# Kernel tuning notes

Measured on AMD Instinct MI355X. Metric: run time of the kernel, lower is better.

Reference implementation:

```python
import jax, jax.numpy as jnp
import numpy as np

N, E = 100000, 1600000
IN_C, OUT_C, H, EDGE_DIM = 128, 64, 2, 4
NEG_SLOPE = 0.2
LN_EPS = 1e-5


def setup_inputs() -> dict:
    key = jax.random.key(0)
    ks = jax.random.split(key, 12)
    s = 1.0 / np.sqrt(IN_C)
    inp = {
        "x": jax.random.normal(ks[0], (N, IN_C), jnp.float32),
        "edge_index": jax.random.randint(ks[1], (2, E), 0, N, jnp.int64),
        "edge_attr": jax.random.normal(ks[2], (E, EDGE_DIM), jnp.float32),
        "W": jax.random.normal(ks[3], (IN_C, H * OUT_C), jnp.float32) * s,
        "att_src": jax.random.normal(ks[4], (H, OUT_C), jnp.float32) * s,
        "att_dst": jax.random.normal(ks[5], (H, OUT_C), jnp.float32) * s,
        "W_edge": jax.random.normal(ks[6], (EDGE_DIM, H * OUT_C), jnp.float32) * 0.5,
        "att_edge": jax.random.normal(ks[7], (H, OUT_C), jnp.float32) * s,
        "bias": jnp.zeros((OUT_C,), jnp.float32),
        "gamma": jnp.ones((OUT_C,), jnp.float32),
        "beta": jnp.zeros((OUT_C,), jnp.float32),
    }
    return inp


def reference(x, edge_index, edge_attr, W, att_src, att_dst, W_edge, att_edge, bias, gamma, beta):
    n = x.shape[0]
    src, dst = edge_index[0], edge_index[1]
    # shared src/dst linear (PyG GATConv with single input tensor)
    h = (x @ W).reshape(n, H, OUT_C)                       # [N,H,C]
    a_src = jnp.einsum("nhc,hc->nh", h, att_src)          # [N,H]
    a_dst = jnp.einsum("nhc,hc->nh", h, att_dst)          # [N,H]
    e = (edge_attr @ W_edge).reshape(-1, H, OUT_C)         # [E,H,C]
    a_edge = jnp.einsum("ehc,hc->eh", e, att_edge)        # [E,H]
    alpha = jax.nn.leaky_relu(a_src[src] + a_dst[dst] + a_edge, NEG_SLOPE)  # [E,H]
    # segment softmax over edges grouped by destination node
    amax = jax.ops.segment_max(alpha, dst, num_segments=n)
    ex = jnp.exp(alpha - amax[dst])
    denom = jax.ops.segment_sum(ex, dst, num_segments=n)
    w = ex / (denom[dst] + 1e-16)                          # [E,H]
    msg = h[src] * w[:, :, None]                           # [E,H,C]
    out = jax.ops.segment_sum(msg, dst, num_segments=n)    # [N,H,C]
    out = out.mean(axis=1) + bias                          # concat=False -> head mean
    # LayerNorm + ReLU
    mu = out.mean(-1, keepdims=True)
    var = ((out - mu) ** 2).mean(-1, keepdims=True)
    out = (out - mu) * jax.lax.rsqrt(var + LN_EPS) * gamma + beta
    return jax.nn.relu(out)
```

## Files before the change

kernel.cpp:

```cpp
#include <hip/hip_runtime.h>
#include <hip/hip_fp16.h>
#include <math.h>

#define IN_C 128
#define HC   128
#define OUT_C 64
#define NEG_SLOPE 0.2f
#define LN_EPS 1e-5f
#define CHUNK 4096
#define BSH   8
#define BMSK  255
#define NBMAX 512
#define NB2MAX 1024

typedef __attribute__((ext_vector_type(8))) _Float16 f16x8;
typedef __attribute__((ext_vector_type(4))) float f32x4;

__device__ inline unsigned h2pack(float a, float b) {
    __half2 h = __floats2half2_rn(a, b);
    return *reinterpret_cast<unsigned*>(&h);
}

__global__ __launch_bounds__(256) void k_pre(const float* __restrict__ W,
                                             const float* __restrict__ W_edge,
                                             const float* __restrict__ att_edge,
                                             const int* __restrict__ ei_dst,
                                             unsigned short* __restrict__ WhT,
                                             float* __restrict__ V,
                                             int* __restrict__ off,
                                             int E, int NB, int PB) {
    __shared__ int hist[NBMAX];
    int b = blockIdx.x, t = threadIdx.x;
    if (b < 8) {
        #pragma unroll
        for (int i = 0; i < 8; ++i) {
            int idx = b * 2048 + i * 256 + t;
            int k = idx >> 7, col = idx & 127;
            __half hh = __float2half_rn(W[idx]);
            WhT[col * 128 + k] = *reinterpret_cast<unsigned short*>(&hh);
        }
        return;
    }
    if (b == 8) {
        if (t < 8) {
            int d = t >> 1, h = t & 1;
            float s = 0.f;
            for (int c = 0; c < 64; ++c)
                s += W_edge[d * HC + h * 64 + c] * att_edge[h * 64 + c];
            V[d * 2 + h] = s;
        }
        return;
    }
    int pb = b - 9;
    for (int i = t; i < NB; i += 256) hist[i] = 0;
    __syncthreads();
    int base = pb * CHUNK;
    int lim = E - base; if (lim > CHUNK) lim = CHUNK;
    if (lim == CHUNK) {
        #pragma unroll
        for (int u = 0; u < 4; ++u) {
            int4 v = *(const int4*)&ei_dst[base + u * 1024 + t * 4];
            atomicAdd(&hist[v.x >> BSH], 1);
            atomicAdd(&hist[v.y >> BSH], 1);
            atomicAdd(&hist[v.z >> BSH], 1);
            atomicAdd(&hist[v.w >> BSH], 1);
        }
    } else {
        for (int i = t; i < lim; i += 256)
            atomicAdd(&hist[ei_dst[base + i] >> BSH], 1);
    }
    __syncthreads();
    for (int i = t; i < NB; i += 256)
        off[(size_t)i * PB + pb] = hist[i];
}

__global__ __launch_bounds__(256) void k_scan(int* __restrict__ off,
                                              int* __restrict__ bsum, int nS) {
    __shared__ int sm[256];
    int t = threadIdx.x;
    int base = blockIdx.x * 1024 + t * 4;
    int v0 = 0, v1 = 0, v2 = 0, v3 = 0;
    if (base + 0 < nS) v0 = off[base + 0];
    if (base + 1 < nS) v1 = off[base + 1];
    if (base + 2 < nS) v2 = off[base + 2];
    if (base + 3 < nS) v3 = off[base + 3];
    int s = v0 + v1 + v2 + v3;
    sm[t] = s;
    __syncthreads();
    for (int o = 1; o < 256; o <<= 1) {
        int u = (t >= o) ? sm[t - o] : 0;
        __syncthreads();
        sm[t] += u;
        __syncthreads();
    }
    int excl = sm[t] - s;
    if (base + 0 < nS) off[base + 0] = excl;
    if (base + 1 < nS) off[base + 1] = excl + v0;
    if (base + 2 < nS) off[base + 2] = excl + v0 + v1;
    if (base + 3 < nS) off[base + 3] = excl + v0 + v1 + v2;
    if (t == 255) bsum[blockIdx.x] = sm[255];
}

__device__ inline void scan_bsum(const int* __restrict__ bsum, int nb2,
                                 int* bs, int* sm, int t) {
    int v0 = (4 * t + 0 < nb2) ? bsum[4 * t + 0] : 0;
    int v1 = (4 * t + 1 < nb2) ? bsum[4 * t + 1] : 0;
    int v2 = (4 * t + 2 < nb2) ? bsum[4 * t + 2] : 0;
    int v3 = (4 * t + 3 < nb2) ? bsum[4 * t + 3] : 0;
    int s = v0 + v1 + v2 + v3;
    sm[t] = s;
    __syncthreads();
    for (int o = 1; o < 256; o <<= 1) {
        int u = (t >= o) ? sm[t - o] : 0;
        __syncthreads();
        sm[t] += u;
        __syncthreads();
    }
    int excl = sm[t] - s;
    bs[4 * t + 0] = excl;
    bs[4 * t + 1] = excl + v0;
    bs[4 * t + 2] = excl + v0 + v1;
    bs[4 * t + 3] = excl + v0 + v1 + v2;
    __syncthreads();
}

__global__ __launch_bounds__(256) void k_fused(
        const float* __restrict__ x,
        const unsigned short* __restrict__ WhT,
        const float* __restrict__ attS, const float* __restrict__ attD,
        unsigned* __restrict__ hb,
        float* __restrict__ a_src, float* __restrict__ a_dst, int M,
        const int* __restrict__ ei, const float* __restrict__ ea,
        const float* __restrict__ V,
        const int* __restrict__ off, const int* __restrict__ bsum,
        int* __restrict__ bsum2, uint2* __restrict__ pA,
        int E, int NB, int PB, int nb2, int GB) {
    __shared__ unsigned xb[64 * 64];
    const int t = threadIdx.x;
    const int bid = blockIdx.x;
    const int r5 = bid % 5, g5 = bid / 5;

    if (r5 == 4) {
        int* cur = (int*)xb;
        int* bs  = (int*)xb + NBMAX;
        int* sm  = (int*)xb + NBMAX + NB2MAX;
        int pb = g5;
        scan_bsum(bsum, nb2, bs, sm, t);
        if (pb == 0)
            for (int i = t; i < nb2; i += 256) bsum2[i] = bs[i];
        for (int i = t; i < NB; i += 256) {
            size_t oi = (size_t)i * PB + pb;
            cur[i] = off[oi] + bs[(int)(oi >> 10)];
        }
        __syncthreads();
        float v0 = V[0], v1 = V[1], v2 = V[2], v3 = V[3];
        float v4 = V[4], v5 = V[5], v6 = V[6], v7 = V[7];
        int base = pb * CHUNK;
        int lim = E - base; if (lim > CHUNK) lim = CHUNK;
        if (lim == CHUNK) {
            #pragma unroll
            for (int h = 0; h < 2; ++h) {
                int e0 = base + h * 2048 + t;
                int sA[8], dA[8];
                #pragma unroll
                for (int k = 0; k < 8; ++k) {
                    sA[k] = ei[e0 + k * 256];
                    dA[k] = ei[E + e0 + k * 256];
                }
                float4 aA[8];
                #pragma unroll
                for (int k = 0; k < 8; ++k)
                    aA[k] = ((const float4*)ea)[e0 + k * 256];
                #pragma unroll
                for (int k = 0; k < 8; ++k) {
                    float ae0 = aA[k].x * v0 + aA[k].y * v2 + aA[k].z * v4 + aA[k].w * v6;
                    float ae1 = aA[k].x * v1 + aA[k].y * v3 + aA[k].z * v5 + aA[k].w * v7;
                    int slot = atomicAdd(&cur[dA[k] >> BSH], 1);
                    pA[slot] = make_uint2(
                        (unsigned)sA[k] | ((unsigned)(dA[k] & BMSK) << 17),
                        h2pack(ae0, ae1));
                }
            }
        } else {
            for (int i = t; i < lim; i += 256) {
                int e = base + i;
                int s = ei[e], d = ei[E + e];
                float4 a = ((const float4*)ea)[e];
                float ae0 = a.x * v0 + a.y * v2 + a.z * v4 + a.w * v6;
                float ae1 = a.x * v1 + a.y * v3 + a.z * v5 + a.w * v7;
                int slot = atomicAdd(&cur[d >> BSH], 1);
                pA[slot] = make_uint2((unsigned)s | ((unsigned)(d & BMSK) << 17),
                                      h2pack(ae0, ae1));
            }
        }
        return;
    }

    const int gid = g5 * 4 + r5;
    if (gid >= GB) return;
    const int brow = gid * 64;
    const float4* x4 = (const float4*)x;
    #pragma unroll
    for (int i = 0; i < 8; ++i) {
        int idx = i * 256 + t;
        int row = idx >> 5, c4 = idx & 31;
        float4 v = make_float4(0.f, 0.f, 0.f, 0.f);
        if (brow + row < M) v = x4[(size_t)(brow + row) * 32 + c4];
        unsigned lo = h2pack(v.x, v.y), hi = h2pack(v.z, v.w);
        int byte = row * 256 + ((c4 * 8) ^ ((row & 7) << 4));
        *(uint2*)((char*)xb + byte) = make_uint2(lo, hi);
    }
    __syncthreads();

    const int w = t >> 6, lane = t & 63;
    const int col = lane & 15, qr = lane >> 4;
    f32x4 acc[8];
    #pragma unroll
    for (int ct = 0; ct < 8; ++ct) acc[ct] = (f32x4){0.f, 0.f, 0.f, 0.f};

    const int arow = w * 16 + col;
    #pragma unroll
    for (int ks = 0; ks < 4; ++ks) {
        int abyte = arow * 256 + ((ks * 64 + qr * 16) ^ ((arow & 7) << 4));
        f16x8 af = *(const f16x8*)((const char*)xb + abyte);
        #pragma unroll
        for (int ct = 0; ct < 8; ++ct) {
            f16x8 bfr = *(const f16x8*)&WhT[(size_t)(ct * 16 + col) * 128 + ks * 32 + qr * 8];
            acc[ct] = __builtin_amdgcn_mfma_f32_16x16x32_f16(af, bfr, acc[ct], 0, 0, 0);
        }
    }

    float pS0[4], pS1[4], pD0[4], pD1[4];
    #pragma unroll
    for (int r = 0; r < 4; ++r) { pS0[r] = pS1[r] = pD0[r] = pD1[r] = 0.f; }
    #pragma unroll
    for (int ct = 0; ct < 8; ++ct) {
        float s = attS[ct * 16 + col], d = attD[ct * 16 + col];
        #pragma unroll
        for (int r = 0; r < 4; ++r) {
            float a = acc[ct][r];
            if (ct < 4) { pS0[r] += a * s; pD0[r] += a * d; }
            else        { pS1[r] += a * s; pD1[r] += a * d; }
        }
    }
    #pragma unroll
    for (int m = 1; m < 16; m <<= 1) {
        #pragma unroll
        for (int r = 0; r < 4; ++r) {
            pS0[r] += __shfl_xor(pS0[r], m);
            pS1[r] += __shfl_xor(pS1[r], m);
            pD0[r] += __shfl_xor(pD0[r], m);
            pD1[r] += __shfl_xor(pD1[r], m);
        }
    }
    #pragma unroll
    for (int r = 0; r < 4; ++r) {
        int grow = brow + w * 16 + qr * 4 + r;
        if (grow < M) {
            if (col == 0) {
                a_src[2 * grow + 0] = pS0[r];
                a_src[2 * grow + 1] = pS1[r];
                a_dst[2 * grow + 0] = pD0[r];
                a_dst[2 * grow + 1] = pD1[r];
            }
            #pragma unroll
            for (int ct = 0; ct < 4; ++ct)
                hb[(size_t)grow * 64 + ct * 16 + col] =
                    h2pack(acc[ct][r], acc[ct + 4][r]);
        }
    }
}

__global__ __launch_bounds__(256) void k_csr(const uint2* __restrict__ pA,
                                             const int* __restrict__ off,
                                             const int* __restrict__ bsum2,
                                             const float* __restrict__ a_src,
                                             const float* __restrict__ a_dst,
                                             int* __restrict__ rowptr,
                                             uint2* __restrict__ payload,
                                             int M, int E, int NB, int PB) {
    __shared__ int cnt[256];
    __shared__ int sc[256];
    __shared__ int cur[256];
    __shared__ float2 adl[256];
    int b = blockIdx.x, t = threadIdx.x;
    int n0 = b << BSH;
    int nloc = M - n0; if (nloc > 256) nloc = 256;

    size_t o0 = (size_t)b * PB;
    int s0 = off[o0] + bsum2[(int)(o0 >> 10)];
    int s1 = E;
    if (b + 1 < NB) {
        size_t o1 = (size_t)(b + 1) * PB;
        s1 = off[o1] + bsum2[(int)(o1 >> 10)];
    }
    cnt[t] = 0;
    if (t < nloc) adl[t] = ((const float2*)a_dst)[n0 + t];
    __syncthreads();

    for (int i = s0 + t; i < s1; i += 256)
        atomicAdd(&cnt[(pA[i].x >> 17) & BMSK], 1);
    __syncthreads();
    int c = cnt[t];
    sc[t] = c;
    __syncthreads();
    for (int o = 1; o < 256; o <<= 1) {
        int u = (t >= o) ? sc[t - o] : 0;
        __syncthreads();
        sc[t] += u;
        __syncthreads();
    }
    {
        int base = s0 + sc[t] - c;
        cur[t] = base;
        if (t < nloc) rowptr[n0 + t] = base;
    }
    if (b == NB - 1 && t == 0) rowptr[M] = E;
    __syncthreads();
    for (int i = s0 + t; i < s1; i += 256) {
        uint2 p = pA[i];
        int src = p.x & 0x1FFFF;
        int dl = (p.x >> 17) & BMSK;
        __half2 aeh = *reinterpret_cast<__half2*>(&p.y);
        float2 as = ((const float2*)a_src)[src];
        float2 ad = adl[dl];
        float al0 = as.x + ad.x + __low2float(aeh);
        al0 = al0 > 0.f ? al0 : NEG_SLOPE * al0;
        float al1 = as.y + ad.y + __high2float(aeh);
        al1 = al1 > 0.f ? al1 : NEG_SLOPE * al1;
        int pos = atomicAdd(&cur[dl], 1);
        payload[pos] = make_uint2((unsigned)src,
                                  h2pack(__expf(al0), __expf(al1)));
    }
}

__global__ __launch_bounds__(256) void k_gather(const uint2* __restrict__ payload,
                                                const int* __restrict__ rowptr,
                                                const unsigned* __restrict__ hb,
                                                const float* __restrict__ bias,
                                                const float* __restrict__ gamma,
                                                const float* __restrict__ beta,
                                                float* __restrict__ out, int M) {
    __shared__ uint2 stg[4][64];
    int w = threadIdx.x >> 6, lane = threadIdx.x & 63;
    int n = blockIdx.x * 4 + w;
    if (n >= M) return;
    int beg = rowptr[n], end = rowptr[n + 1];
    float acc0 = 0.f, acc1 = 0.f, pe0 = 0.f, pe1 = 0.f;

    for (int base = beg; base < end; base += 64) {
        int cnt = end - base; if (cnt > 64) cnt = 64;
        uint2 p = make_uint2(0u, 0u);
        if (lane < cnt) p = payload[base + lane];
        stg[w][lane] = p;
        {
            __half2 he = *reinterpret_cast<__half2*>(&p.y);
            pe0 += __low2float(he);
            pe1 += __high2float(he);
        }
        int j = 0;
        for (; j + 8 <= cnt; j += 8) {
            uint2 q0 = stg[w][j + 0], q1 = stg[w][j + 1];
            uint2 q2 = stg[w][j + 2], q3 = stg[w][j + 3];
            uint2 q4 = stg[w][j + 4], q5 = stg[w][j + 5];
            uint2 q6 = stg[w][j + 6], q7 = stg[w][j + 7];
            int s0 = __builtin_amdgcn_readfirstlane((int)q0.x);
            int s1 = __builtin_amdgcn_readfirstlane((int)q1.x);
            int s2 = __builtin_amdgcn_readfirstlane((int)q2.x);
            int s3 = __builtin_amdgcn_readfirstlane((int)q3.x);
            int s4 = __builtin_amdgcn_readfirstlane((int)q4.x);
            int s5 = __builtin_amdgcn_readfirstlane((int)q5.x);
            int s6 = __builtin_amdgcn_readfirstlane((int)q6.x);
            int s7 = __builtin_amdgcn_readfirstlane((int)q7.x);
            unsigned h0 = (hb + (size_t)s0 * 64)[lane];
            unsigned h1 = (hb + (size_t)s1 * 64)[lane];
            unsigned h2 = (hb + (size_t)s2 * 64)[lane];
            unsigned h3 = (hb + (size_t)s3 * 64)[lane];
            unsigned h4 = (hb + (size_t)s4 * 64)[lane];
            unsigned h5 = (hb + (size_t)s5 * 64)[lane];
            unsigned h6 = (hb + (size_t)s6 * 64)[lane];
            unsigned h7 = (hb + (size_t)s7 * 64)[lane];
            __half2 e0 = *reinterpret_cast<__half2*>(&q0.y);
            __half2 e1 = *reinterpret_cast<__half2*>(&q1.y);
            __half2 e2 = *reinterpret_cast<__half2*>(&q2.y);
            __half2 e3 = *reinterpret_cast<__half2*>(&q3.y);
            __half2 e4 = *reinterpret_cast<__half2*>(&q4.y);
            __half2 e5 = *reinterpret_cast<__half2*>(&q5.y);
            __half2 e6 = *reinterpret_cast<__half2*>(&q6.y);
            __half2 e7 = *reinterpret_cast<__half2*>(&q7.y);
            __half2 g0 = *reinterpret_cast<__half2*>(&h0);
            __half2 g1 = *reinterpret_cast<__half2*>(&h1);
            __half2 g2 = *reinterpret_cast<__half2*>(&h2);
            __half2 g3 = *reinterpret_cast<__half2*>(&h3);
            __half2 g4 = *reinterpret_cast<__half2*>(&h4);
            __half2 g5 = *reinterpret_cast<__half2*>(&h5);
            __half2 g6 = *reinterpret_cast<__half2*>(&h6);
            __half2 g7 = *reinterpret_cast<__half2*>(&h7);
            acc0 += __low2float(e0)  * __low2float(g0);
            acc1 += __high2float(e0) * __high2float(g0);
            acc0 += __low2float(e1)  * __low2float(g1);
            acc1 += __high2float(e1) * __high2float(g1);
            acc0 += __low2float(e2)  * __low2float(g2);
            acc1 += __high2float(e2) * __high2float(g2);
            acc0 += __low2float(e3)  * __low2float(g3);
            acc1 += __high2float(e3) * __high2float(g3);
            acc0 += __low2float(e4)  * __low2float(g4);
            acc1 += __high2float(e4) * __high2float(g4);
            acc0 += __low2float(e5)  * __low2float(g5);
            acc1 += __high2float(e5) * __high2float(g5);
            acc0 += __low2float(e6)  * __low2float(g6);
            acc1 += __high2float(e6) * __high2float(g6);
            acc0 += __low2float(e7)  * __low2float(g7);
            acc1 += __high2float(e7) * __high2float(g7);
        }
        for (; j + 4 <= cnt; j += 4) {
            uint2 q0 = stg[w][j + 0], q1 = stg[w][j + 1];
            uint2 q2 = stg[w][j + 2], q3 = stg[w][j + 3];
            int s0 = __builtin_amdgcn_readfirstlane((int)q0.x);
            int s1 = __builtin_amdgcn_readfirstlane((int)q1.x);
            int s2 = __builtin_amdgcn_readfirstlane((int)q2.x);
            int s3 = __builtin_amdgcn_readfirstlane((int)q3.x);
            unsigned h0 = (hb + (size_t)s0 * 64)[lane];
            unsigned h1 = (hb + (size_t)s1 * 64)[lane];
            unsigned h2 = (hb + (size_t)s2 * 64)[lane];
            unsigned h3 = (hb + (size_t)s3 * 64)[lane];
            __half2 e0 = *reinterpret_cast<__half2*>(&q0.y);
            __half2 e1 = *reinterpret_cast<__half2*>(&q1.y);
            __half2 e2 = *reinterpret_cast<__half2*>(&q2.y);
            __half2 e3 = *reinterpret_cast<__half2*>(&q3.y);
            __half2 g0 = *reinterpret_cast<__half2*>(&h0);
            __half2 g1 = *reinterpret_cast<__half2*>(&h1);
            __half2 g2 = *reinterpret_cast<__half2*>(&h2);
            __half2 g3 = *reinterpret_cast<__half2*>(&h3);
            acc0 += __low2float(e0)  * __low2float(g0);
            acc1 += __high2float(e0) * __high2float(g0);
            acc0 += __low2float(e1)  * __low2float(g1);
            acc1 += __high2float(e1) * __high2float(g1);
            acc0 += __low2float(e2)  * __low2float(g2);
            acc1 += __high2float(e2) * __high2float(g2);
            acc0 += __low2float(e3)  * __low2float(g3);
            acc1 += __high2float(e3) * __high2float(g3);
        }
        for (; j < cnt; ++j) {
            uint2 q0 = stg[w][j];
            int s0 = __builtin_amdgcn_readfirstlane((int)q0.x);
            unsigned h0 = (hb + (size_t)s0 * 64)[lane];
            __half2 e0 = *reinterpret_cast<__half2*>(&q0.y);
            __half2 g0 = *reinterpret_cast<__half2*>(&h0);
            acc0 += __low2float(e0)  * __low2float(g0);
            acc1 += __high2float(e0) * __high2float(g0);
        }
    }

    float d0 = pe0, d1 = pe1;
    #pragma unroll
    for (int m = 32; m; m >>= 1) {
        d0 += __shfl_xor(d0, m);
        d1 += __shfl_xor(d1, m);
    }

    float o = 0.5f * (acc0 / (d0 + 1e-16f) + acc1 / (d1 + 1e-16f)) + bias[lane];
    float mu = o;
    #pragma unroll
    for (int m = 32; m; m >>= 1) mu += __shfl_xor(mu, m);
    mu *= (1.f / 64.f);
    float c = o - mu;
    float v = c * c;
    #pragma unroll
    for (int m = 32; m; m >>= 1) v += __shfl_xor(v, m);
    v *= (1.f / 64.f);
    float y = c * rsqrtf(v + LN_EPS) * gamma[lane] + beta[lane];
    out[(size_t)n * OUT_C + lane] = fmaxf(y, 0.f);
}

extern "C" void kernel_launch(void* const* d_in, const int* in_sizes, int n_in,
                              void* d_out, int out_size, void* d_ws, size_t ws_size,
                              hipStream_t stream) {
    const float* x     = (const float*)d_in[0];
    const int*   ei    = (const int*)d_in[1];
    const float* ea    = (const float*)d_in[2];
    const float* W     = (const float*)d_in[3];
    const float* attS  = (const float*)d_in[4];
    const float* attD  = (const float*)d_in[5];
    const float* We    = (const float*)d_in[6];
    const float* attE  = (const float*)d_in[7];
    const float* bias  = (const float*)d_in[8];
    const float* gamma = (const float*)d_in[9];
    const float* beta  = (const float*)d_in[10];

    const int M  = in_sizes[0] / IN_C;
    const int E  = in_sizes[1] / 2;
    const int NB = (M + BMSK) >> BSH;
    const int PB = (E + CHUNK - 1) / CHUNK;
    const int nS = NB * PB;
    const int nb2 = (nS + 1023) / 1024;
    const int GB = (M + 63) / 64;

    char* ws = (char*)d_ws;
    size_t woff = 0;
    auto alloc = [&](size_t bytes) -> void* {
        void* p = ws + woff;
        woff += (bytes + 255) & ~(size_t)255;
        return p;
    };
    unsigned*       hb     = (unsigned*)      alloc((size_t)M * 64 * 4);
    float*          a_src  = (float*)         alloc((size_t)M * 2 * 4);
    float*          a_dst  = (float*)         alloc((size_t)M * 2 * 4);
    int*            off    = (int*)           alloc((size_t)nS * 4);
    int*            bsum   = (int*)           alloc((size_t)nb2 * 4);
    int*            bsum2  = (int*)           alloc((size_t)nb2 * 4);
    int*            rowptr = (int*)           alloc((size_t)(M + 1) * 4);
    uint2*          pA     = (uint2*)         alloc((size_t)E * 8);
    uint2*          payload= (uint2*)         alloc((size_t)E * 8);
    unsigned short* WhT    = (unsigned short*)alloc(128 * 128 * 2);
    float*          V      = (float*)         alloc(32);

    k_pre<<<9 + PB, 256, 0, stream>>>(W, We, attE, ei + E, WhT, V, off, E, NB, PB);
    k_scan<<<nb2, 256, 0, stream>>>(off, bsum, nS);
    k_fused<<<5 * PB, 256, 0, stream>>>(x, WhT, attS, attD, hb, a_src, a_dst, M,
                                        ei, ea, V, off, bsum, bsum2, pA,
                                        E, NB, PB, nb2, GB);
    k_csr<<<NB, 256, 0, stream>>>(pA, off, bsum2, a_src, a_dst, rowptr, payload,
                                  M, E, NB, PB);
    k_gather<<<(M + 3) / 4, 256, 0, stream>>>(payload, rowptr, hb, bias, gamma, beta,
                                              (float*)d_out, M);
}
```

Measured before the change: 143.8 us.

## Precompute attention logits via folded W·att vectors in k_pre; move exp to scatter

Folds att_src/att_dst into W to get four 128-length vectors, and computes a_src/a_dst per node directly from fp32 x inside the histogram kernel. The partition stage of k_fused then gathers a_src/a_dst and stores exp(leaky_relu(logit)) in the payload. k_csr becomes a plain permute without random a_src reads. This moves the random gather earlier and cuts the reduction epilogue from the MFMA path, at the cost of an extra full read of x in k_pre and random a_src/a_dst gathers in the scatter pass.

```diff
diff --git a/kernel.cpp b/kernel.cpp
--- a/kernel.cpp
+++ b/kernel.cpp
@@ -24,12 +24,18 @@
 __global__ __launch_bounds__(256) void k_pre(const float* __restrict__ W,
                                              const float* __restrict__ W_edge,
                                              const float* __restrict__ att_edge,
+                                             const float* __restrict__ attS,
+                                             const float* __restrict__ attD,
+                                             const float* __restrict__ x,
                                              const int* __restrict__ ei_dst,
                                              unsigned short* __restrict__ WhT,
                                              float* __restrict__ V,
                                              int* __restrict__ off,
-                                             int E, int NB, int PB) {
+                                             float* __restrict__ a_src,
+                                             float* __restrict__ a_dst,
+                                             int E, int M, int NB, int PB) {
     __shared__ int hist[NBMAX];
+    __shared__ float wsv0[128], wsv1[128], wdv0[128], wdv1[128];
     int b = blockIdx.x, t = threadIdx.x;
     if (b < 8) {
         #pragma unroll
@@ -52,26 +58,63 @@
         return;
     }
     int pb = b - 9;
+
     for (int i = t; i < NB; i += 256) hist[i] = 0;
-    __syncthreads();
-    int base = pb * CHUNK;
-    int lim = E - base; if (lim > CHUNK) lim = CHUNK;
-    if (lim == CHUNK) {
-        #pragma unroll
-        for (int u = 0; u < 4; ++u) {
-            int4 v = *(const int4*)&ei_dst[base + u * 1024 + t * 4];
-            atomicAdd(&hist[v.x >> BSH], 1);
-            atomicAdd(&hist[v.y >> BSH], 1);
-            atomicAdd(&hist[v.z >> BSH], 1);
-            atomicAdd(&hist[v.w >> BSH], 1);
-        }
-    } else {
-        for (int i = t; i < lim; i += 256)
-            atomicAdd(&hist[ei_dst[base + i] >> BSH], 1);
-    }
-    __syncthreads();
-    for (int i = t; i < NB; i += 256)
-        off[(size_t)i * PB + pb] = hist[i];
+    if (t < 128) {
+        const float* wr = W + t * 128;
+        float s0 = 0.f, s1 = 0.f, d0 = 0.f, d1 = 0.f;
+        for (int c = 0; c < 64; ++c) {
+            float w0 = wr[c], w1 = wr[64 + c];
+            s0 += w0 * attS[c];      s1 += w1 * attS[64 + c];
+            d0 += w0 * attD[c];      d1 += w1 * attD[64 + c];
+        }
+        wsv0[t] = s0; wsv1[t] = s1; wdv0[t] = d0; wdv1[t] = d1;
+    }
+    __syncthreads();
+
+    if (pb < PB) {
+        int base = pb * CHUNK;
+        int lim = E - base; if (lim > CHUNK) lim = CHUNK;
+        if (lim == CHUNK) {
+            #pragma unroll
+            for (int u = 0; u < 4; ++u) {
+                int4 v = *(const int4*)&ei_dst[base + u * 1024 + t * 4];
+                atomicAdd(&hist[v.x >> BSH], 1);
+                atomicAdd(&hist[v.y >> BSH], 1);
+                atomicAdd(&hist[v.z >> BSH], 1);
+                atomicAdd(&hist[v.w >> BSH], 1);
+            }
+        } else {
+            for (int i = t; i < lim; i += 256)
+                atomicAdd(&hist[ei_dst[base + i] >> BSH], 1);
+        }
+    }
+    {
+        int n = pb * 256 + t;
+        if (pb < NB && n < M) {
+            const float4* xr4 = (const float4*)(x + (size_t)n * 128);
+            float s0 = 0.f, s1 = 0.f, d0 = 0.f, d1 = 0.f;
+            #pragma unroll 8
+            for (int q = 0; q < 32; ++q) {
+                float4 xv = xr4[q];
+                int k = q * 4;
+                s0 += xv.x * wsv0[k]     + xv.y * wsv0[k + 1]
+                    + xv.z * wsv0[k + 2] + xv.w * wsv0[k + 3];
+                s1 += xv.x * wsv1[k]     + xv.y * wsv1[k + 1]
+                    + xv.z * wsv1[k + 2] + xv.w * wsv1[k + 3];
+                d0 += xv.x * wdv0[k]     + xv.y * wdv0[k + 1]
+                    + xv.z * wdv0[k + 2] + xv.w * wdv0[k + 3];
+                d1 += xv.x * wdv1[k]     + xv.y * wdv1[k + 1]
+                    + xv.z * wdv1[k + 2] + xv.w * wdv1[k + 3];
+            }
+            ((float2*)a_src)[n] = make_float2(s0, s1);
+            ((float2*)a_dst)[n] = make_float2(d0, d1);
+        }
+    }
+    __syncthreads();
+    if (pb < PB)
+        for (int i = t; i < NB; i += 256)
+            off[(size_t)i * PB + pb] = hist[i];
 }
 
 __global__ __launch_bounds__(256) void k_scan(int* __restrict__ off,
@@ -127,11 +170,10 @@
 __global__ __launch_bounds__(256) void k_fused(
         const float* __restrict__ x,
         const unsigned short* __restrict__ WhT,
-        const float* __restrict__ attS, const float* __restrict__ attD,
-        unsigned* __restrict__ hb,
-        float* __restrict__ a_src, float* __restrict__ a_dst, int M,
+        unsigned* __restrict__ hb, int M,
         const int* __restrict__ ei, const float* __restrict__ ea,
         const float* __restrict__ V,
+        const float* __restrict__ a_src, const float* __restrict__ a_dst,
         const int* __restrict__ off, const int* __restrict__ bsum,
         int* __restrict__ bsum2, uint2* __restrict__ pA,
         int E, int NB, int PB, int nb2, int GB) {
@@ -171,14 +213,24 @@
                 #pragma unroll
                 for (int k = 0; k < 8; ++k)
                     aA[k] = ((const float4*)ea)[e0 + k * 256];
+                float2 asA[8], adA[8];
+                #pragma unroll
+                for (int k = 0; k < 8; ++k) {
+                    asA[k] = ((const float2*)a_src)[sA[k]];
+                    adA[k] = ((const float2*)a_dst)[dA[k]];
+                }
                 #pragma unroll
                 for (int k = 0; k < 8; ++k) {
                     float ae0 = aA[k].x * v0 + aA[k].y * v2 + aA[k].z * v4 + aA[k].w * v6;
                     float ae1 = aA[k].x * v1 + aA[k].y * v3 + aA[k].z * v5 + aA[k].w * v7;
+                    float al0 = asA[k].x + adA[k].x + ae0;
+                    al0 = al0 > 0.f ? al0 : NEG_SLOPE * al0;
+                    float al1 = asA[k].y + adA[k].y + ae1;
+                    al1 = al1 > 0.f ? al1 : NEG_SLOPE * al1;
                     int slot = atomicAdd(&cur[dA[k] >> BSH], 1);
                     pA[slot] = make_uint2(
                         (unsigned)sA[k] | ((unsigned)(dA[k] & BMSK) << 17),
-                        h2pack(ae0, ae1));
+                        h2pack(__expf(al0), __expf(al1)));
                 }
             }
         } else {
@@ -188,9 +240,13 @@
                 float4 a = ((const float4*)ea)[e];
                 float ae0 = a.x * v0 + a.y * v2 + a.z * v4 + a.w * v6;
                 float ae1 = a.x * v1 + a.y * v3 + a.z * v5 + a.w * v7;
+                float2 as = ((const float2*)a_src)[s];
+                float2 ad = ((const float2*)a_dst)[d];
+                float al0 = as.x + ad.x + ae0; al0 = al0 > 0.f ? al0 : NEG_SLOPE * al0;
+                float al1 = as.y + ad.y + ae1; al1 = al1 > 0.f ? al1 : NEG_SLOPE * al1;
                 int slot = atomicAdd(&cur[d >> BSH], 1);
                 pA[slot] = make_uint2((unsigned)s | ((unsigned)(d & BMSK) << 17),
-                                      h2pack(ae0, ae1));
+                                      h2pack(__expf(al0), __expf(al1)));
             }
         }
         return;
@@ -230,39 +286,10 @@
         }
     }
 
-    float pS0[4], pS1[4], pD0[4], pD1[4];
-    #pragma unroll
-    for (int r = 0; r < 4; ++r) { pS0[r] = pS1[r] = pD0[r] = pD1[r] = 0.f; }
-    #pragma unroll
-    for (int ct = 0; ct < 8; ++ct) {
-        float s = attS[ct * 16 + col], d = attD[ct * 16 + col];
-        #pragma unroll
-        for (int r = 0; r < 4; ++r) {
-            float a = acc[ct][r];
-            if (ct < 4) { pS0[r] += a * s; pD0[r] += a * d; }
-            else        { pS1[r] += a * s; pD1[r] += a * d; }
-        }
-    }
-    #pragma unroll
-    for (int m = 1; m < 16; m <<= 1) {
-        #pragma unroll
-        for (int r = 0; r < 4; ++r) {
-            pS0[r] += __shfl_xor(pS0[r], m);
-            pS1[r] += __shfl_xor(pS1[r], m);
-            pD0[r] += __shfl_xor(pD0[r], m);
-            pD1[r] += __shfl_xor(pD1[r], m);
-        }
-    }
     #pragma unroll
     for (int r = 0; r < 4; ++r) {
         int grow = brow + w * 16 + qr * 4 + r;
         if (grow < M) {
-            if (col == 0) {
-                a_src[2 * grow + 0] = pS0[r];
-                a_src[2 * grow + 1] = pS1[r];
-                a_dst[2 * grow + 0] = pD0[r];
-                a_dst[2 * grow + 1] = pD1[r];
-            }
             #pragma unroll
             for (int ct = 0; ct < 4; ++ct)
                 hb[(size_t)grow * 64 + ct * 16 + col] =
@@ -274,15 +301,12 @@
 __global__ __launch_bounds__(256) void k_csr(const uint2* __restrict__ pA,
                                              const int* __restrict__ off,
                                              const int* __restrict__ bsum2,
-                                             const float* __restrict__ a_src,
-                                             const float* __restrict__ a_dst,
                                              int* __restrict__ rowptr,
                                              uint2* __restrict__ payload,
                                              int M, int E, int NB, int PB) {
     __shared__ int cnt[256];
     __shared__ int sc[256];
     __shared__ int cur[256];
-    __shared__ float2 adl[256];
     int b = blockIdx.x, t = threadIdx.x;
     int n0 = b << BSH;
     int nloc = M - n0; if (nloc > 256) nloc = 256;
@@ -295,7 +319,6 @@
         s1 = off[o1] + bsum2[(int)(o1 >> 10)];
     }
     cnt[t] = 0;
-    if (t < nloc) adl[t] = ((const float2*)a_dst)[n0 + t];
     __syncthreads();
 
     for (int i = s0 + t; i < s1; i += 256)
@@ -319,18 +342,9 @@
     __syncthreads();
     for (int i = s0 + t; i < s1; i += 256) {
         uint2 p = pA[i];
-        int src = p.x & 0x1FFFF;
         int dl = (p.x >> 17) & BMSK;
-        __half2 aeh = *reinterpret_cast<__half2*>(&p.y);
-        float2 as = ((const float2*)a_src)[src];
-        float2 ad = adl[dl];
-        float al0 = as.x + ad.x + __low2float(aeh);
-        al0 = al0 > 0.f ? al0 : NEG_SLOPE * al0;
-        float al1 = as.y + ad.y + __high2float(aeh);
-        al1 = al1 > 0.f ? al1 : NEG_SLOPE * al1;
         int pos = atomicAdd(&cur[dl], 1);
-        payload[pos] = make_uint2((unsigned)src,
-                                  h2pack(__expf(al0), __expf(al1)));
+        payload[pos] = make_uint2(p.x & 0x1FFFF, p.y);
     }
 }
 
@@ -495,6 +509,7 @@
     const int nS = NB * PB;
     const int nb2 = (nS + 1023) / 1024;
     const int GB = (M + 63) / 64;
+    const int PREB = (PB > NB ? PB : NB);
 
     char* ws = (char*)d_ws;
     size_t woff = 0;
@@ -515,13 +530,12 @@
     unsigned short* WhT    = (unsigned short*)alloc(128 * 128 * 2);
     float*          V      = (float*)         alloc(32);
 
-    k_pre<<<9 + PB, 256, 0, stream>>>(W, We, attE, ei + E, WhT, V, off, E, NB, PB);
+    k_pre<<<9 + PREB, 256, 0, stream>>>(W, We, attE, attS, attD, x, ei + E,
+                                        WhT, V, off, a_src, a_dst, E, M, NB, PB);
     k_scan<<<nb2, 256, 0, stream>>>(off, bsum, nS);
-    k_fused<<<5 * PB, 256, 0, stream>>>(x, WhT, attS, attD, hb, a_src, a_dst, M,
-                                        ei, ea, V, off, bsum, bsum2, pA,
-                                        E, NB, PB, nb2, GB);
-    k_csr<<<NB, 256, 0, stream>>>(pA, off, bsum2, a_src, a_dst, rowptr, payload,
-                                  M, E, NB, PB);
+    k_fused<<<5 * PB, 256, 0, stream>>>(x, WhT, hb, M, ei, ea, V, a_src, a_dst,
+                                        off, bsum, bsum2, pA, E, NB, PB, nb2, GB);
+    k_csr<<<NB, 256, 0, stream>>>(pA, off, bsum2, rowptr, payload, M, E, NB, PB);
     k_gather<<<(M + 3) / 4, 256, 0, stream>>>(payload, rowptr, hb, bias, gamma, beta,
                                               (float*)d_out, M);
 }
```

Measured after the change: 173.9 us. +20.9%, slower.

## Fuse offset scan with GEMM kernel and compute attention exp during partition

Applied to the files above, without the earlier changes.

The chunk-offset scan now runs as extra blocks inside the node GEMM kernel, and the edge partition becomes its own kernel launched after it. Because a_src and a_dst are then ready, the partition computes the leaky-relu and exp of the attention logit and stores it in the payload. The CSR kernel only copies the payload instead of gathering a_src per edge. This removes one launch and moves the random a_src gather to a phase with better memory-level parallelism, but it loses the overlap of partitioning with the GEMM and adds random a_dst reads.

```diff
diff --git a/kernel.cpp b/kernel.cpp
--- a/kernel.cpp
+++ b/kernel.cpp
@@ -74,131 +74,48 @@
         off[(size_t)i * PB + pb] = hist[i];
 }
 
-__global__ __launch_bounds__(256) void k_scan(int* __restrict__ off,
-                                              int* __restrict__ bsum, int nS) {
-    __shared__ int sm[256];
-    int t = threadIdx.x;
-    int base = blockIdx.x * 1024 + t * 4;
-    int v0 = 0, v1 = 0, v2 = 0, v3 = 0;
-    if (base + 0 < nS) v0 = off[base + 0];
-    if (base + 1 < nS) v1 = off[base + 1];
-    if (base + 2 < nS) v2 = off[base + 2];
-    if (base + 3 < nS) v3 = off[base + 3];
-    int s = v0 + v1 + v2 + v3;
-    sm[t] = s;
-    __syncthreads();
-    for (int o = 1; o < 256; o <<= 1) {
-        int u = (t >= o) ? sm[t - o] : 0;
-        __syncthreads();
-        sm[t] += u;
-        __syncthreads();
-    }
-    int excl = sm[t] - s;
-    if (base + 0 < nS) off[base + 0] = excl;
-    if (base + 1 < nS) off[base + 1] = excl + v0;
-    if (base + 2 < nS) off[base + 2] = excl + v0 + v1;
-    if (base + 3 < nS) off[base + 3] = excl + v0 + v1 + v2;
-    if (t == 255) bsum[blockIdx.x] = sm[255];
-}
-
-__device__ inline void scan_bsum(const int* __restrict__ bsum, int nb2,
-                                 int* bs, int* sm, int t) {
-    int v0 = (4 * t + 0 < nb2) ? bsum[4 * t + 0] : 0;
-    int v1 = (4 * t + 1 < nb2) ? bsum[4 * t + 1] : 0;
-    int v2 = (4 * t + 2 < nb2) ? bsum[4 * t + 2] : 0;
-    int v3 = (4 * t + 3 < nb2) ? bsum[4 * t + 3] : 0;
-    int s = v0 + v1 + v2 + v3;
-    sm[t] = s;
-    __syncthreads();
-    for (int o = 1; o < 256; o <<= 1) {
-        int u = (t >= o) ? sm[t - o] : 0;
-        __syncthreads();
-        sm[t] += u;
-        __syncthreads();
-    }
-    int excl = sm[t] - s;
-    bs[4 * t + 0] = excl;
-    bs[4 * t + 1] = excl + v0;
-    bs[4 * t + 2] = excl + v0 + v1;
-    bs[4 * t + 3] = excl + v0 + v1 + v2;
-    __syncthreads();
-}
-
-__global__ __launch_bounds__(256) void k_fused(
-        const float* __restrict__ x,
-        const unsigned short* __restrict__ WhT,
-        const float* __restrict__ attS, const float* __restrict__ attD,
-        unsigned* __restrict__ hb,
-        float* __restrict__ a_src, float* __restrict__ a_dst, int M,
-        const int* __restrict__ ei, const float* __restrict__ ea,
-        const float* __restrict__ V,
-        const int* __restrict__ off, const int* __restrict__ bsum,
-        int* __restrict__ bsum2, uint2* __restrict__ pA,
-        int E, int NB, int PB, int nb2, int GB) {
+__global__ __launch_bounds__(256) void k_mid(const float* __restrict__ x,
+                                             const unsigned short* __restrict__ WhT,
+                                             const float* __restrict__ attS,
+                                             const float* __restrict__ attD,
+                                             unsigned* __restrict__ hb,
+                                             float* __restrict__ a_src,
+                                             float* __restrict__ a_dst, int M,
+                                             int* __restrict__ off,
+                                             int* __restrict__ bsum,
+                                             int nS, int GB) {
     __shared__ unsigned xb[64 * 64];
     const int t = threadIdx.x;
     const int bid = blockIdx.x;
-    const int r5 = bid % 5, g5 = bid / 5;
-
-    if (r5 == 4) {
-        int* cur = (int*)xb;
-        int* bs  = (int*)xb + NBMAX;
-        int* sm  = (int*)xb + NBMAX + NB2MAX;
-        int pb = g5;
-        scan_bsum(bsum, nb2, bs, sm, t);
-        if (pb == 0)
-            for (int i = t; i < nb2; i += 256) bsum2[i] = bs[i];
-        for (int i = t; i < NB; i += 256) {
-            size_t oi = (size_t)i * PB + pb;
-            cur[i] = off[oi] + bs[(int)(oi >> 10)];
-        }
+
+    if (bid >= GB) {
+        int* sm = (int*)xb;
+        int blk = bid - GB;
+        int base = blk * 1024 + t * 4;
+        int v0 = 0, v1 = 0, v2 = 0, v3 = 0;
+        if (base + 0 < nS) v0 = off[base + 0];
+        if (base + 1 < nS) v1 = off[base + 1];
+        if (base + 2 < nS) v2 = off[base + 2];
+        if (base + 3 < nS) v3 = off[base + 3];
+        int s = v0 + v1 + v2 + v3;
+        sm[t] = s;
         __syncthreads();
-        float v0 = V[0], v1 = V[1], v2 = V[2], v3 = V[3];
-        float v4 = V[4], v5 = V[5], v6 = V[6], v7 = V[7];
-        int base = pb * CHUNK;
-        int lim = E - base; if (lim > CHUNK) lim = CHUNK;
-        if (lim == CHUNK) {
-            #pragma unroll
-            for (int h = 0; h < 2; ++h) {
-                int e0 = base + h * 2048 + t;
-                int sA[8], dA[8];
-                #pragma unroll
-                for (int k = 0; k < 8; ++k) {
-                    sA[k] = ei[e0 + k * 256];
-                    dA[k] = ei[E + e0 + k * 256];
-                }
-                float4 aA[8];
-                #pragma unroll
-                for (int k = 0; k < 8; ++k)
-                    aA[k] = ((const float4*)ea)[e0 + k * 256];
-                #pragma unroll
-                for (int k = 0; k < 8; ++k) {
-                    float ae0 = aA[k].x * v0 + aA[k].y * v2 + aA[k].z * v4 + aA[k].w * v6;
-                    float ae1 = aA[k].x * v1 + aA[k].y * v3 + aA[k].z * v5 + aA[k].w * v7;
-                    int slot = atomicAdd(&cur[dA[k] >> BSH], 1);
-                    pA[slot] = make_uint2(
-                        (unsigned)sA[k] | ((unsigned)(dA[k] & BMSK) << 17),
-                        h2pack(ae0, ae1));
-                }
-            }
-        } else {
-            for (int i = t; i < lim; i += 256) {
-                int e = base + i;
-                int s = ei[e], d = ei[E + e];
-                float4 a = ((const float4*)ea)[e];
-                float ae0 = a.x * v0 + a.y * v2 + a.z * v4 + a.w * v6;
-                float ae1 = a.x * v1 + a.y * v3 + a.z * v5 + a.w * v7;
-                int slot = atomicAdd(&cur[d >> BSH], 1);
-                pA[slot] = make_uint2((unsigned)s | ((unsigned)(d & BMSK) << 17),
-                                      h2pack(ae0, ae1));
-            }
-        }
+        for (int o = 1; o < 256; o <<= 1) {
+            int u = (t >= o) ? sm[t - o] : 0;
+            __syncthreads();
+            sm[t] += u;
+            __syncthreads();
+        }
+        int excl = sm[t] - s;
+        if (base + 0 < nS) off[base + 0] = excl;
+        if (base + 1 < nS) off[base + 1] = excl + v0;
+        if (base + 2 < nS) off[base + 2] = excl + v0 + v1;
+        if (base + 3 < nS) off[base + 3] = excl + v0 + v1 + v2;
+        if (t == 255) bsum[blk] = sm[255];
         return;
     }
 
-    const int gid = g5 * 4 + r5;
-    if (gid >= GB) return;
-    const int brow = gid * 64;
+    const int brow = bid * 64;
     const float4* x4 = (const float4*)x;
     #pragma unroll
     for (int i = 0; i < 8; ++i) {
@@ -271,18 +188,118 @@
     }
 }
 
+__device__ inline void scan_bsum(const int* __restrict__ bsum, int nb2,
+                                 int* bs, int* sm, int t) {
+    int v0 = (4 * t + 0 < nb2) ? bsum[4 * t + 0] : 0;
+    int v1 = (4 * t + 1 < nb2) ? bsum[4 * t + 1] : 0;
+    int v2 = (4 * t + 2 < nb2) ? bsum[4 * t + 2] : 0;
+    int v3 = (4 * t + 3 < nb2) ? bsum[4 * t + 3] : 0;
+    int s = v0 + v1 + v2 + v3;
+    sm[t] = s;
+    __syncthreads();
+    for (int o = 1; o < 256; o <<= 1) {
+        int u = (t >= o) ? sm[t - o] : 0;
+        __syncthreads();
+        sm[t] += u;
+        __syncthreads();
+    }
+    int excl = sm[t] - s;
+    bs[4 * t + 0] = excl;
+    bs[4 * t + 1] = excl + v0;
+    bs[4 * t + 2] = excl + v0 + v1;
+    bs[4 * t + 3] = excl + v0 + v1 + v2;
+    __syncthreads();
+}
+
+__global__ __launch_bounds__(256) void k_part(const int* __restrict__ ei,
+                                              const float* __restrict__ ea,
+                                              const float* __restrict__ V,
+                                              const float* __restrict__ a_src,
+                                              const float* __restrict__ a_dst,
+                                              const int* __restrict__ off,
+                                              const int* __restrict__ bsum,
+                                              int* __restrict__ bsum2,
+                                              uint2* __restrict__ pA,
+                                              int E, int NB, int PB, int nb2) {
+    __shared__ int cur[NBMAX];
+    __shared__ int bs[NB2MAX];
+    __shared__ int sm[256];
+    int pb = blockIdx.x, t = threadIdx.x;
+
+    scan_bsum(bsum, nb2, bs, sm, t);
+    if (pb == 0)
+        for (int i = t; i < nb2; i += 256) bsum2[i] = bs[i];
+
+    for (int i = t; i < NB; i += 256) {
+        size_t oi = (size_t)i * PB + pb;
+        cur[i] = off[oi] + bs[(int)(oi >> 10)];
+    }
+    __syncthreads();
+    float v0 = V[0], v1 = V[1], v2 = V[2], v3 = V[3];
+    float v4 = V[4], v5 = V[5], v6 = V[6], v7 = V[7];
+    int base = pb * CHUNK;
+    int lim = E - base; if (lim > CHUNK) lim = CHUNK;
+
+    if (lim == CHUNK) {
+        #pragma unroll
+        for (int h = 0; h < 2; ++h) {
+            int e0 = base + h * 2048 + t;
+            int sA[8], dA[8];
+            #pragma unroll
+            for (int k = 0; k < 8; ++k) {
+                sA[k] = ei[e0 + k * 256];
+                dA[k] = ei[E + e0 + k * 256];
+            }
+            float4 aA[8];
+            #pragma unroll
+            for (int k = 0; k < 8; ++k) aA[k] = ((const float4*)ea)[e0 + k * 256];
+            float2 asA[8], adA[8];
+            #pragma unroll
+            for (int k = 0; k < 8; ++k) {
+                asA[k] = ((const float2*)a_src)[sA[k]];
+                adA[k] = ((const float2*)a_dst)[dA[k]];
+            }
+            #pragma unroll
+            for (int k = 0; k < 8; ++k) {
+                float ae0 = aA[k].x * v0 + aA[k].y * v2 + aA[k].z * v4 + aA[k].w * v6;
+                float ae1 = aA[k].x * v1 + aA[k].y * v3 + aA[k].z * v5 + aA[k].w * v7;
+                float al0 = asA[k].x + adA[k].x + ae0;
+                al0 = al0 > 0.f ? al0 : NEG_SLOPE * al0;
+                float al1 = asA[k].y + adA[k].y + ae1;
+                al1 = al1 > 0.f ? al1 : NEG_SLOPE * al1;
+                int slot = atomicAdd(&cur[dA[k] >> BSH], 1);
+                pA[slot] = make_uint2(
+                    (unsigned)sA[k] | ((unsigned)(dA[k] & BMSK) << 17),
+                    h2pack(__expf(al0), __expf(al1)));
+            }
+        }
+    } else {
+        for (int i = t; i < lim; i += 256) {
+            int e = base + i;
+            int s = ei[e], d = ei[E + e];
+            float4 a = ((const float4*)ea)[e];
+            float ae0 = a.x * v0 + a.y * v2 + a.z * v4 + a.w * v6;
+            float ae1 = a.x * v1 + a.y * v3 + a.z * v5 + a.w * v7;
+            float2 as = ((const float2*)a_src)[s];
+            float2 ad = ((const float2*)a_dst)[d];
+            float al0 = as.x + ad.x + ae0; al0 = al0 > 0.f ? al0 : NEG_SLOPE * al0;
+            float al1 = as.y + ad.y + ae1; al1 = al1 > 0.f ? al1 : NEG_SLOPE * al1;
+            int slot = atomicAdd(&cur[d >> BSH], 1);
+            pA[slot] = make_uint2((unsigned)s | ((unsigned)(d & BMSK) << 17),
+                                  h2pack(__expf(al0), __expf(al1)));
+        }
+    }
+}
+
 __global__ __launch_bounds__(256) void k_csr(const uint2* __restrict__ pA,
                                              const int* __restrict__ off,
                                              const int* __restrict__ bsum2,
-                                             const float* __restrict__ a_src,
-                                             const float* __restrict__ a_dst,
                                              int* __restrict__ rowptr,
                                              uint2* __restrict__ payload,
                                              int M, int E, int NB, int PB) {
     __shared__ int cnt[256];
     __shared__ int sc[256];
     __shared__ int cur[256];
-    __shared__ float2 adl[256];
     int b = blockIdx.x, t = threadIdx.x;
     int n0 = b << BSH;
     int nloc = M - n0; if (nloc > 256) nloc = 256;
@@ -295,7 +312,6 @@
         s1 = off[o1] + bsum2[(int)(o1 >> 10)];
     }
     cnt[t] = 0;
-    if (t < nloc) adl[t] = ((const float2*)a_dst)[n0 + t];
     __syncthreads();
 
     for (int i = s0 + t; i < s1; i += 256)
@@ -319,18 +335,9 @@
     __syncthreads();
     for (int i = s0 + t; i < s1; i += 256) {
         uint2 p = pA[i];
-        int src = p.x & 0x1FFFF;
         int dl = (p.x >> 17) & BMSK;
-        __half2 aeh = *reinterpret_cast<__half2*>(&p.y);
-        float2 as = ((const float2*)a_src)[src];
-        float2 ad = adl[dl];
-        float al0 = as.x + ad.x + __low2float(aeh);
-        al0 = al0 > 0.f ? al0 : NEG_SLOPE * al0;
-        float al1 = as.y + ad.y + __high2float(aeh);
-        al1 = al1 > 0.f ? al1 : NEG_SLOPE * al1;
         int pos = atomicAdd(&cur[dl], 1);
-        payload[pos] = make_uint2((unsigned)src,
-                                  h2pack(__expf(al0), __expf(al1)));
+        payload[pos] = make_uint2(p.x & 0x1FFFF, p.y);
     }
 }
 
@@ -516,12 +523,11 @@
     float*          V      = (float*)         alloc(32);
 
     k_pre<<<9 + PB, 256, 0, stream>>>(W, We, attE, ei + E, WhT, V, off, E, NB, PB);
-    k_scan<<<nb2, 256, 0, stream>>>(off, bsum, nS);
-    k_fused<<<5 * PB, 256, 0, stream>>>(x, WhT, attS, attD, hb, a_src, a_dst, M,
-                                        ei, ea, V, off, bsum, bsum2, pA,
-                                        E, NB, PB, nb2, GB);
-    k_csr<<<NB, 256, 0, stream>>>(pA, off, bsum2, a_src, a_dst, rowptr, payload,
-                                  M, E, NB, PB);
+    k_mid<<<GB + nb2, 256, 0, stream>>>(x, WhT, attS, attD, hb, a_src, a_dst, M,
+                                        off, bsum, nS, GB);
+    k_part<<<PB, 256, 0, stream>>>(ei, ea, V, a_src, a_dst, off, bsum, bsum2,
+                                   pA, E, NB, PB, nb2);
+    k_csr<<<NB, 256, 0, stream>>>(pA, off, bsum2, rowptr, payload, M, E, NB, PB);
     k_gather<<<(M + 3) / 4, 256, 0, stream>>>(payload, rowptr, hb, bias, gamma, beta,
                                               (float*)d_out, M);
 }
```

New measurement: 159.0 us. +10.6%, slower.
